# Performance work log

Measured on AMD Instinct MI355X. Metric: run time of the kernel, lower is better.

The kernel has to match this reference:

```python
import jax, jax.numpy as jnp
import numpy as np

WS = (4, 4, 4)          # window size (s, h, w)
NUM_HEADS = 6
DIM = 192               # kv channels C
CS = 2                  # channel_scale; q/out channels = DIM // CS
B = 256                 # num_windows * batch


def _rel_pos_index(ws):
    """Reproduces the module's relative_position_index buffer (shape [8shw, 2shw])."""
    s, h, w = ws
    cs = np.repeat(np.arange(s), 2)
    ch = np.repeat(np.arange(h), 2)
    cw = np.repeat(np.arange(w), 2)
    coords = np.stack(np.meshgrid(cs, ch, cw, indexing='ij'))   # (3, 2s, 2h, 2w)
    cf = coords.reshape(3, -1)                                   # (3, T), T = 8shw
    rel = cf[:, :, None] - cf[:, None, :]                        # (3, T, T)
    rel = rel[:, :, ::4]                                         # (3, T, T//4)
    rel = np.ascontiguousarray(rel.transpose(1, 2, 0))           # (T, T//4, 3)
    rel[:, :, 0] += s - 1
    rel[:, :, 1] += h - 1
    rel[:, :, 2] += w - 1
    rel[:, :, 0] *= 3 * h - 1
    rel[:, :, 1] *= 2 * h - 1
    return rel.sum(-1).astype(np.int32)                          # (T, T//4)


def setup_inputs() -> dict:
    key = jax.random.key(0)
    ks = jax.random.split(key, 9)
    s, h, w = WS
    qN = 8 * s * h * w          # 512 query tokens per window
    N = qN // 4                 # 128 key/value tokens per window
    C = DIM
    qC = DIM // CS
    table_len = (4 * s - 1) * (4 * h - 1) * (4 * w - 1)
    return {
        'kv': jax.random.normal(ks[0], (B, N, C), jnp.float32),
        'q': jax.random.normal(ks[1], (B, qN, qC), jnp.float32),
        'w_kv': jax.random.normal(ks[2], (C, 2 * C), jnp.float32) * 0.02,
        'b_kv': jnp.zeros((2 * C,), jnp.float32),
        'w_q': jax.random.normal(ks[3], (qC, C), jnp.float32) * 0.02,
        'b_q': jnp.zeros((C,), jnp.float32),
        'w_proj': jax.random.normal(ks[4], (C, qC), jnp.float32) * 0.02,
        'b_proj': jnp.zeros((qC,), jnp.float32),
        'bias_table': jax.random.normal(ks[5], (table_len, NUM_HEADS), jnp.float32) * 0.02,
        'rel_index': jnp.asarray(_rel_pos_index(WS)),
    }


def reference(kv, q, w_kv, b_kv, w_q, b_q, w_proj, b_proj, bias_table, rel_index):
    B_, N, C = kv.shape
    d = C // NUM_HEADS
    scale = d ** -0.5
    # project kv -> k, v : (B_, nH, N, d)
    kvp = (kv @ w_kv + b_kv).reshape(B_, N, 2, NUM_HEADS, d)
    k = kvp[:, :, 0].transpose(0, 2, 1, 3)
    v = kvp[:, :, 1].transpose(0, 2, 1, 3)
    # project q : (B_, nH, qN, d), pre-scaled
    qp = (q @ w_q + b_q).reshape(B_, -1, NUM_HEADS, d).transpose(0, 2, 1, 3) * scale
    attn = jnp.einsum('bhqd,bhkd->bhqk', qp, k)          # (B_, nH, qN, N)
    bias = bias_table[rel_index]                          # (qN, N, nH) gather
    attn = attn + bias.transpose(2, 0, 1)[None]           # + (1, nH, qN, N)
    attn = jax.nn.softmax(attn, axis=-1)
    out = jnp.einsum('bhqk,bhkd->bhqd', attn, v)          # (B_, nH, qN, d)
    out = out.transpose(0, 2, 1, 3).reshape(B_, -1, C)    # (B_, qN, C)
    return out @ w_proj + b_proj                          # (B_, qN, C//CS)
```

## Files before the change

### kernel.cpp

```cpp
#include <hip/hip_runtime.h>
#include <hip/hip_bf16.h>

#define B_    256
#define NKV   128
#define NQ    512
#define CDIM  192
#define QCDIM 96
#define NH    6
#define DH    32
#define SCALE 0.17677669529663687f

typedef __hip_bfloat16 bf16;
typedef __attribute__((ext_vector_type(8))) short s16x8;
typedef __attribute__((ext_vector_type(4))) float f32x4;
#define MFMA16(a, b, c) __builtin_amdgcn_mfma_f32_16x16x32_bf16(a, b, c, 0, 0, 0)

#define OFF_BIAS  0
#define OFF_WKVT  1572864
#define OFF_WQT   (OFF_WKVT + 147456)
#define OFF_WPT   (OFF_WQT + 36864)
#define OFF_O     2097152

#define LDS_K    0
#define LDS_VT   10240
#define LDS_STG  18944
#define LDS_P    18944
#define LDS_WKV  53760
#define LDS_WQ   53760
#define LDS_SQ   60416
#define LDS_TOT  79360

__global__ __launch_bounds__(256)
void precomp_bias(const float* __restrict__ bias_table, const int* __restrict__ rel_index,
                  float* __restrict__ biasM)
{
    const int i = blockIdx.x * 256 + threadIdx.x;
    const int h   = i >> 16;
    const int rem = i & 65535;
    biasM[i] = bias_table[rel_index[rem] * NH + h];
}

__global__ __launch_bounds__(256)
void precomp_w(const float* __restrict__ w_kv, const float* __restrict__ w_q,
               const float* __restrict__ w_proj,
               bf16* __restrict__ wkvT, bf16* __restrict__ wqT, bf16* __restrict__ wpT)
{
    const int i = blockIdx.x * 256 + threadIdx.x;
    if (i < NH * 64 * CDIM) {
        const int k = i % CDIM, jh = i / CDIM;
        const int j = jh & 63, h = jh >> 6;
        const int col = (j < DH) ? (h * DH + j) : (CDIM + h * DH + (j - DH));
        wkvT[i] = __float2bfloat16(w_kv[k * (2 * CDIM) + col]);
    } else if (i < NH * 64 * CDIM + NH * DH * QCDIM) {
        const int i2 = i - NH * 64 * CDIM;
        const int k = i2 % QCDIM, jh = i2 / QCDIM;
        const int j = jh & 31, h = jh >> 5;
        wqT[i2] = __float2bfloat16(w_q[k * CDIM + h * DH + j] * SCALE);
    } else {
        const int i3 = i - NH * 64 * CDIM - NH * DH * QCDIM;
        const int k = i3 % CDIM, n = i3 / CDIM;
        wpT[i3] = __float2bfloat16(w_proj[k * QCDIM + n]);
    }
}

__global__ __launch_bounds__(512, 4)
void attn_fused(const float* __restrict__ kv, const float* __restrict__ q,
                const float* __restrict__ b_kv, const float* __restrict__ b_q,
                const char* __restrict__ wsro, bf16* __restrict__ O)
{
    __shared__ __align__(16) char smem[LDS_TOT];
    bf16* sK   = (bf16*)(smem + LDS_K);
    bf16* sVT  = (bf16*)(smem + LDS_VT);
    bf16* sStg = (bf16*)(smem + LDS_STG);
    bf16* sP   = (bf16*)(smem + LDS_P);
    bf16* sWkv = (bf16*)(smem + LDS_WKV);
    bf16* sWq  = (bf16*)(smem + LDS_WQ);
    bf16* sQ   = (bf16*)(smem + LDS_SQ);

    const int b = blockIdx.x, h = blockIdx.y;
    const int t = threadIdx.x;
    const int wave = t >> 6, lane = t & 63, quad = lane >> 4, l16 = lane & 15;
    const f32x4 ZV = {0.f, 0.f, 0.f, 0.f};

    const float* biasM  = (const float*)(wsro + OFF_BIAS);
    const bf16*  wkvT_g = (const bf16*)(wsro + OFF_WKVT) + h * 64 * CDIM;
    const bf16*  wqT_g  = (const bf16*)(wsro + OFF_WQT) + h * DH * QCDIM;

    for (int f = t; f < 1536; f += 512) {
        const int j = f / 24, k8 = f % 24;
        *(uint4*)&sWkv[j * 200 + k8 * 8] = *(const uint4*)&wkvT_g[j * CDIM + k8 * 8];
    }

    f32x4 acc[4];
    #pragma unroll
    for (int i = 0; i < 4; ++i) acc[i] = ZV;

    for (int half = 0; half < 2; ++half) {
        for (int f = t; f < 3072; f += 512) {
            const int r = f / 24, c4 = f % 24;
            const float4 v = *(const float4*)&kv[((size_t)b * NKV + r) * CDIM + half * QCDIM + c4 * 4];
            __align__(8) bf16 tmp[4] = {__float2bfloat16(v.x), __float2bfloat16(v.y),
                                        __float2bfloat16(v.z), __float2bfloat16(v.w)};
            *(uint2*)&sStg[r * 104 + c4 * 4] = *(uint2*)tmp;
        }
        __syncthreads();
        #pragma unroll
        for (int kk = 0; kk < 3; ++kk) {
            const s16x8 a = *(const s16x8*)&sStg[(wave * 16 + l16) * 104 + kk * 32 + quad * 8];
            #pragma unroll
            for (int tl = 0; tl < 4; ++tl) {
                const s16x8 bb = *(const s16x8*)&sWkv[(tl * 16 + l16) * 200 + half * QCDIM + kk * 32 + quad * 8];
                acc[tl] = MFMA16(a, bb, acc[tl]);
            }
        }
        __syncthreads();
    }
    #pragma unroll
    for (int tl = 0; tl < 4; ++tl) {
        const int j = tl * 16 + l16;
        const float bkv = (j < DH) ? b_kv[h * DH + j] : b_kv[CDIM + h * DH + (j - DH)];
        #pragma unroll
        for (int r = 0; r < 4; ++r) {
            const int m = wave * 16 + quad * 4 + r;
            const float v = acc[tl][r] + bkv;
            if (j < DH) sK[m * 40 + j] = __float2bfloat16(v);
            else        sVT[(j - DH) * 136 + m] = __float2bfloat16(v);
        }
    }
    for (int f = t; f < 384; f += 512) {
        const int j = f / 12, k8 = f % 12;
        *(uint4*)&sWq[j * 104 + k8 * 8] = *(const uint4*)&wqT_g[j * QCDIM + k8 * 8];
    }

    for (int qc = 0; qc < 4; ++qc) {
        __syncthreads();
        for (int f = t; f < 3072; f += 512) {
            const int r = f / 24, c4 = f % 24;
            const float4 v = *(const float4*)&q[((size_t)b * NQ + qc * 128 + r) * QCDIM + c4 * 4];
            __align__(8) bf16 tmp[4] = {__float2bfloat16(v.x), __float2bfloat16(v.y),
                                        __float2bfloat16(v.z), __float2bfloat16(v.w)};
            *(uint2*)&sStg[r * 104 + c4 * 4] = *(uint2*)tmp;
        }
        __syncthreads();

        f32x4 qacc[2];
        qacc[0] = ZV; qacc[1] = ZV;
        #pragma unroll
        for (int kk = 0; kk < 3; ++kk) {
            const s16x8 a = *(const s16x8*)&sStg[(wave * 16 + l16) * 104 + kk * 32 + quad * 8];
            #pragma unroll
            for (int tl = 0; tl < 2; ++tl) {
                const s16x8 bb = *(const s16x8*)&sWq[(tl * 16 + l16) * 104 + kk * 32 + quad * 8];
                qacc[tl] = MFMA16(a, bb, qacc[tl]);
            }
        }
        #pragma unroll
        for (int tl = 0; tl < 2; ++tl) {
            const int cc = tl * 16 + l16;
            const float bq = b_q[h * DH + cc] * SCALE;
            #pragma unroll
            for (int r = 0; r < 4; ++r)
                sQ[(wave * 16 + quad * 4 + r) * 40 + cc] = __float2bfloat16(qacc[tl][r] + bq);
        }
        __syncthreads();

        f32x4 sacc[8];
        {
            const s16x8 a = *(const s16x8*)&sQ[(wave * 16 + l16) * 40 + quad * 8];
            #pragma unroll
            for (int tl = 0; tl < 8; ++tl) {
                const s16x8 bb = *(const s16x8*)&sK[(tl * 16 + l16) * 40 + quad * 8];
                sacc[tl] = MFMA16(a, bb, ZV);
            }
        }
        #pragma unroll
        for (int r = 0; r < 4; ++r) {
            const int qrow = qc * 128 + wave * 16 + quad * 4 + r;
            const float* brow = biasM + (((size_t)h * NQ + qrow) << 7) + l16;
            float v[8];
            float mx = -1e30f;
            #pragma unroll
            for (int tl = 0; tl < 8; ++tl) {
                v[tl] = sacc[tl][r] + brow[tl * 16];
                mx = fmaxf(mx, v[tl]);
            }
            #pragma unroll
            for (int off = 1; off < 16; off <<= 1) mx = fmaxf(mx, __shfl_xor(mx, off));
            float sum = 0.f;
            #pragma unroll
            for (int tl = 0; tl < 8; ++tl) { v[tl] = __expf(v[tl] - mx); sum += v[tl]; }
            #pragma unroll
            for (int off = 1; off < 16; off <<= 1) sum += __shfl_xor(sum, off);
            const float inv = 1.f / sum;
            const int prow = wave * 16 + quad * 4 + r;
            #pragma unroll
            for (int tl = 0; tl < 8; ++tl)
                sP[prow * 136 + tl * 16 + l16] = __float2bfloat16(v[tl] * inv);
        }
        __syncthreads();

        f32x4 oacc[2];
        oacc[0] = ZV; oacc[1] = ZV;
        #pragma unroll
        for (int kk = 0; kk < 4; ++kk) {
            const s16x8 a = *(const s16x8*)&sP[(wave * 16 + l16) * 136 + kk * 32 + quad * 8];
            #pragma unroll
            for (int tl = 0; tl < 2; ++tl) {
                const s16x8 bb = *(const s16x8*)&sVT[(tl * 16 + l16) * 136 + kk * 32 + quad * 8];
                oacc[tl] = MFMA16(a, bb, oacc[tl]);
            }
        }
        #pragma unroll
        for (int tl = 0; tl < 2; ++tl)
            #pragma unroll
            for (int r = 0; r < 4; ++r)
                O[((size_t)(b * NQ + qc * 128 + wave * 16 + quad * 4 + r)) * CDIM
                  + h * DH + tl * 16 + l16] = __float2bfloat16(oacc[tl][r]);
    }
}

__global__ __launch_bounds__(256)
void final_proj(const bf16* __restrict__ O, const bf16* __restrict__ wpT,
                const float* __restrict__ b_proj, float* __restrict__ out)
{
    __shared__ __align__(16) bf16 sO[64 * 200];
    __shared__ __align__(16) bf16 sW[96 * 200];
    const int row0 = blockIdx.x * 64;
    const int t = threadIdx.x;
    const int wave = t >> 6, lane = t & 63, quad = lane >> 4, l16 = lane & 15;
    const f32x4 ZV = {0.f, 0.f, 0.f, 0.f};

    for (int f = t; f < 1536; f += 256) {
        const int r = f / 24, c8 = f % 24;
        *(uint4*)&sO[r * 200 + c8 * 8] = *(const uint4*)&O[((size_t)(row0 + r)) * CDIM + c8 * 8];
    }
    for (int f = t; f < 2304; f += 256) {
        const int r = f / 24, c8 = f % 24;
        *(uint4*)&sW[r * 200 + c8 * 8] = *(const uint4*)&wpT[r * CDIM + c8 * 8];
    }
    __syncthreads();

    f32x4 acc[6];
    #pragma unroll
    for (int i = 0; i < 6; ++i) acc[i] = ZV;
    #pragma unroll
    for (int kk = 0; kk < 6; ++kk) {
        const s16x8 a = *(const s16x8*)&sO[(wave * 16 + l16) * 200 + kk * 32 + quad * 8];
        #pragma unroll
        for (int tl = 0; tl < 6; ++tl) {
            const s16x8 bb = *(const s16x8*)&sW[(tl * 16 + l16) * 200 + kk * 32 + quad * 8];
            acc[tl] = MFMA16(a, bb, acc[tl]);
        }
    }
    #pragma unroll
    for (int tl = 0; tl < 6; ++tl) {
        const float bp = b_proj[tl * 16 + l16];
        #pragma unroll
        for (int r = 0; r < 4; ++r)
            out[(size_t)(row0 + wave * 16 + quad * 4 + r) * QCDIM + tl * 16 + l16] = acc[tl][r] + bp;
    }
}

extern "C" void kernel_launch(void* const* d_in, const int* in_sizes, int n_in,
                              void* d_out, int out_size, void* d_ws, size_t ws_size,
                              hipStream_t stream)
{
    const float* kv       = (const float*)d_in[0];
    const float* q        = (const float*)d_in[1];
    const float* w_kv     = (const float*)d_in[2];
    const float* b_kv     = (const float*)d_in[3];
    const float* w_q      = (const float*)d_in[4];
    const float* b_q      = (const float*)d_in[5];
    const float* w_proj   = (const float*)d_in[6];
    const float* b_proj   = (const float*)d_in[7];
    const float* bias_tab = (const float*)d_in[8];
    const int*   rel_idx  = (const int*)d_in[9];
    char* ws = (char*)d_ws;

    precomp_bias<<<1536, 256, 0, stream>>>(bias_tab, rel_idx, (float*)(ws + OFF_BIAS));
    precomp_w<<<432, 256, 0, stream>>>(w_kv, w_q, w_proj,
                                       (bf16*)(ws + OFF_WKVT), (bf16*)(ws + OFF_WQT),
                                       (bf16*)(ws + OFF_WPT));
    attn_fused<<<dim3(B_, NH), 512, 0, stream>>>(kv, q, b_kv, b_q,
                                                 (const char*)ws, (bf16*)(ws + OFF_O));
    final_proj<<<(B_ * NQ) / 64, 256, 0, stream>>>((const bf16*)(ws + OFF_O),
                                                   (const bf16*)(ws + OFF_WPT),
                                                   b_proj, (float*)d_out);
}
```

Measured before the change: 257.5 us.

## Split KV projection into own kernel and fuse output projection into attention

Moves the K/V projection into a separate proj_kv kernel that writes bf16 K and transposed V to workspace. The attention kernel is reorganised to run one block per (window, query chunk) and loop over all heads, accumulating the output projection in registers. This removes the intermediate O buffer, the final_proj launch, and the q reload per head. The cost is that K, V and weights are read straight from global memory inside the MFMA loops instead of from LDS, and each block now does more serial work across heads.

Result: slower. 343.4 us (+33.3%).

```diff
diff --git a/kernel.cpp b/kernel.cpp
--- a/kernel.cpp
+++ b/kernel.cpp
@@ -19,16 +19,8 @@
 #define OFF_WKVT  1572864
 #define OFF_WQT   (OFF_WKVT + 147456)
 #define OFF_WPT   (OFF_WQT + 36864)
-#define OFF_O     2097152
-
-#define LDS_K    0
-#define LDS_VT   10240
-#define LDS_STG  18944
-#define LDS_P    18944
-#define LDS_WKV  53760
-#define LDS_WQ   53760
-#define LDS_SQ   60416
-#define LDS_TOT  79360
+#define OFF_KP    (OFF_WPT + 36864)
+#define OFF_VT    (OFF_KP + 12582912)
 
 __global__ __launch_bounds__(256)
 void precomp_bias(const float* __restrict__ bias_table, const int* __restrict__ rel_index,
@@ -46,137 +38,138 @@
                bf16* __restrict__ wkvT, bf16* __restrict__ wqT, bf16* __restrict__ wpT)
 {
     const int i = blockIdx.x * 256 + threadIdx.x;
-    if (i < NH * 64 * CDIM) {
-        const int k = i % CDIM, jh = i / CDIM;
-        const int j = jh & 63, h = jh >> 6;
-        const int col = (j < DH) ? (h * DH + j) : (CDIM + h * DH + (j - DH));
-        wkvT[i] = __float2bfloat16(w_kv[k * (2 * CDIM) + col]);
-    } else if (i < NH * 64 * CDIM + NH * DH * QCDIM) {
-        const int i2 = i - NH * 64 * CDIM;
-        const int k = i2 % QCDIM, jh = i2 / QCDIM;
-        const int j = jh & 31, h = jh >> 5;
-        wqT[i2] = __float2bfloat16(w_q[k * CDIM + h * DH + j] * SCALE);
+    if (i < 384 * CDIM) {
+        const int n = i / CDIM, k = i % CDIM;
+        wkvT[i] = __float2bfloat16(w_kv[k * (2 * CDIM) + n]);
+    } else if (i < 384 * CDIM + CDIM * QCDIM) {
+        const int i2 = i - 384 * CDIM;
+        const int n = i2 / QCDIM, k = i2 % QCDIM;
+        wqT[i2] = __float2bfloat16(w_q[k * CDIM + n] * SCALE);
     } else {
-        const int i3 = i - NH * 64 * CDIM - NH * DH * QCDIM;
-        const int k = i3 % CDIM, n = i3 / CDIM;
+        const int i3 = i - 384 * CDIM - CDIM * QCDIM;
+        const int n = i3 / CDIM, k = i3 % CDIM;
         wpT[i3] = __float2bfloat16(w_proj[k * QCDIM + n]);
     }
 }
 
+__global__ __launch_bounds__(512)
+void proj_kv(const float* __restrict__ kv, const float* __restrict__ b_kv,
+             const bf16* __restrict__ wkvT, bf16* __restrict__ Kp, bf16* __restrict__ VTp)
+{
+    __shared__ __align__(16) bf16 sA[128 * 200];
+    const int b = blockIdx.x, t = threadIdx.x;
+    const int w = t >> 6, lane = t & 63, quad = lane >> 4, l16 = lane & 15;
+    const f32x4 ZV = {0.f, 0.f, 0.f, 0.f};
+
+    for (int f = t; f < 6144; f += 512) {
+        const int r = f / 48, c4 = f % 48;
+        const float4 v = *(const float4*)&kv[((size_t)b * NKV + r) * CDIM + c4 * 4];
+        __align__(8) bf16 tmp[4] = {__float2bfloat16(v.x), __float2bfloat16(v.y),
+                                    __float2bfloat16(v.z), __float2bfloat16(v.w)};
+        *(uint2*)&sA[r * 200 + c4 * 4] = *(uint2*)tmp;
+    }
+    __syncthreads();
+
+    f32x4 acc[24];
+    #pragma unroll
+    for (int i = 0; i < 24; ++i) acc[i] = ZV;
+    for (int kk = 0; kk < 6; ++kk) {
+        const s16x8 a = *(const s16x8*)&sA[(w * 16 + l16) * 200 + kk * 32 + quad * 8];
+        #pragma unroll
+        for (int nt = 0; nt < 24; ++nt) {
+            const s16x8 bb = *(const s16x8*)&wkvT[(nt * 16 + l16) * CDIM + kk * 32 + quad * 8];
+            acc[nt] = MFMA16(a, bb, acc[nt]);
+        }
+    }
+    #pragma unroll
+    for (int nt = 0; nt < 24; ++nt) {
+        const int col = nt * 16 + l16;
+        const float bias = b_kv[col];
+        if (nt < 12) {
+            #pragma unroll
+            for (int r = 0; r < 4; ++r) {
+                const int m = w * 16 + quad * 4 + r;
+                Kp[((size_t)b * NKV + m) * CDIM + col] = __float2bfloat16(acc[nt][r] + bias);
+            }
+        } else {
+            const int j = col - CDIM;
+            __align__(8) bf16 tmp[4];
+            #pragma unroll
+            for (int r = 0; r < 4; ++r) tmp[r] = __float2bfloat16(acc[nt][r] + bias);
+            *(uint2*)&VTp[((size_t)b * CDIM + j) * NKV + w * 16 + quad * 4] = *(uint2*)tmp;
+        }
+    }
+}
+
 __global__ __launch_bounds__(512, 4)
-void attn_fused(const float* __restrict__ kv, const float* __restrict__ q,
-                const float* __restrict__ b_kv, const float* __restrict__ b_q,
-                const char* __restrict__ wsro, bf16* __restrict__ O)
-{
-    __shared__ __align__(16) char smem[LDS_TOT];
-    bf16* sK   = (bf16*)(smem + LDS_K);
-    bf16* sVT  = (bf16*)(smem + LDS_VT);
-    bf16* sStg = (bf16*)(smem + LDS_STG);
-    bf16* sP   = (bf16*)(smem + LDS_P);
-    bf16* sWkv = (bf16*)(smem + LDS_WKV);
-    bf16* sWq  = (bf16*)(smem + LDS_WQ);
-    bf16* sQ   = (bf16*)(smem + LDS_SQ);
-
-    const int b = blockIdx.x, h = blockIdx.y;
+void attn_fused(const float* __restrict__ q, const float* __restrict__ b_q,
+                const float* __restrict__ b_proj, const char* __restrict__ wsro,
+                float* __restrict__ out)
+{
+    __shared__ __align__(16) char smem[61440];
+    bf16* sQin = (bf16*)smem;
+    bf16* sP   = (bf16*)(smem + 26624);
+
+    const int b = blockIdx.x, qc = blockIdx.y;
     const int t = threadIdx.x;
-    const int wave = t >> 6, lane = t & 63, quad = lane >> 4, l16 = lane & 15;
+    const int w = t >> 6, lane = t & 63, quad = lane >> 4, l16 = lane & 15;
     const f32x4 ZV = {0.f, 0.f, 0.f, 0.f};
 
-    const float* biasM  = (const float*)(wsro + OFF_BIAS);
-    const bf16*  wkvT_g = (const bf16*)(wsro + OFF_WKVT) + h * 64 * CDIM;
-    const bf16*  wqT_g  = (const bf16*)(wsro + OFF_WQT) + h * DH * QCDIM;
-
-    for (int f = t; f < 1536; f += 512) {
-        const int j = f / 24, k8 = f % 24;
-        *(uint4*)&sWkv[j * 200 + k8 * 8] = *(const uint4*)&wkvT_g[j * CDIM + k8 * 8];
-    }
-
-    f32x4 acc[4];
-    #pragma unroll
-    for (int i = 0; i < 4; ++i) acc[i] = ZV;
-
-    for (int half = 0; half < 2; ++half) {
-        for (int f = t; f < 3072; f += 512) {
-            const int r = f / 24, c4 = f % 24;
-            const float4 v = *(const float4*)&kv[((size_t)b * NKV + r) * CDIM + half * QCDIM + c4 * 4];
-            __align__(8) bf16 tmp[4] = {__float2bfloat16(v.x), __float2bfloat16(v.y),
-                                        __float2bfloat16(v.z), __float2bfloat16(v.w)};
-            *(uint2*)&sStg[r * 104 + c4 * 4] = *(uint2*)tmp;
-        }
-        __syncthreads();
-        #pragma unroll
-        for (int kk = 0; kk < 3; ++kk) {
-            const s16x8 a = *(const s16x8*)&sStg[(wave * 16 + l16) * 104 + kk * 32 + quad * 8];
-            #pragma unroll
-            for (int tl = 0; tl < 4; ++tl) {
-                const s16x8 bb = *(const s16x8*)&sWkv[(tl * 16 + l16) * 200 + half * QCDIM + kk * 32 + quad * 8];
-                acc[tl] = MFMA16(a, bb, acc[tl]);
-            }
-        }
-        __syncthreads();
-    }
-    #pragma unroll
-    for (int tl = 0; tl < 4; ++tl) {
-        const int j = tl * 16 + l16;
-        const float bkv = (j < DH) ? b_kv[h * DH + j] : b_kv[CDIM + h * DH + (j - DH)];
-        #pragma unroll
-        for (int r = 0; r < 4; ++r) {
-            const int m = wave * 16 + quad * 4 + r;
-            const float v = acc[tl][r] + bkv;
-            if (j < DH) sK[m * 40 + j] = __float2bfloat16(v);
-            else        sVT[(j - DH) * 136 + m] = __float2bfloat16(v);
-        }
-    }
-    for (int f = t; f < 384; f += 512) {
-        const int j = f / 12, k8 = f % 12;
-        *(uint4*)&sWq[j * 104 + k8 * 8] = *(const uint4*)&wqT_g[j * QCDIM + k8 * 8];
-    }
-
-    for (int qc = 0; qc < 4; ++qc) {
-        __syncthreads();
-        for (int f = t; f < 3072; f += 512) {
-            const int r = f / 24, c4 = f % 24;
-            const float4 v = *(const float4*)&q[((size_t)b * NQ + qc * 128 + r) * QCDIM + c4 * 4];
-            __align__(8) bf16 tmp[4] = {__float2bfloat16(v.x), __float2bfloat16(v.y),
-                                        __float2bfloat16(v.z), __float2bfloat16(v.w)};
-            *(uint2*)&sStg[r * 104 + c4 * 4] = *(uint2*)tmp;
-        }
-        __syncthreads();
-
+    const float* biasM = (const float*)(wsro + OFF_BIAS);
+    const bf16*  wqT   = (const bf16*)(wsro + OFF_WQT);
+    const bf16*  wpT   = (const bf16*)(wsro + OFF_WPT);
+    const bf16*  Kp    = (const bf16*)(wsro + OFF_KP) + (size_t)b * NKV * CDIM;
+    const bf16*  VTp   = (const bf16*)(wsro + OFF_VT) + (size_t)b * CDIM * NKV;
+
+    for (int f = t; f < 3072; f += 512) {
+        const int r = f / 24, c4 = f % 24;
+        const float4 v = *(const float4*)&q[((size_t)b * NQ + qc * 128 + r) * QCDIM + c4 * 4];
+        __align__(8) bf16 tmp[4] = {__float2bfloat16(v.x), __float2bfloat16(v.y),
+                                    __float2bfloat16(v.z), __float2bfloat16(v.w)};
+        *(uint2*)&sQin[r * 104 + c4 * 4] = *(uint2*)tmp;
+    }
+    __syncthreads();
+
+    bf16* myP = sP + w * 16 * 136;
+
+    f32x4 outacc[6];
+    #pragma unroll
+    for (int i = 0; i < 6; ++i) outacc[i] = ZV;
+
+    for (int h = 0; h < NH; ++h) {
         f32x4 qacc[2];
         qacc[0] = ZV; qacc[1] = ZV;
         #pragma unroll
         for (int kk = 0; kk < 3; ++kk) {
-            const s16x8 a = *(const s16x8*)&sStg[(wave * 16 + l16) * 104 + kk * 32 + quad * 8];
+            const s16x8 a = *(const s16x8*)&sQin[(w * 16 + l16) * 104 + kk * 32 + quad * 8];
             #pragma unroll
             for (int tl = 0; tl < 2; ++tl) {
-                const s16x8 bb = *(const s16x8*)&sWq[(tl * 16 + l16) * 104 + kk * 32 + quad * 8];
+                const s16x8 bb = *(const s16x8*)&wqT[(h * DH + tl * 16 + l16) * QCDIM + kk * 32 + quad * 8];
                 qacc[tl] = MFMA16(a, bb, qacc[tl]);
             }
         }
         #pragma unroll
         for (int tl = 0; tl < 2; ++tl) {
-            const int cc = tl * 16 + l16;
-            const float bq = b_q[h * DH + cc] * SCALE;
+            const float bq = b_q[h * DH + tl * 16 + l16] * SCALE;
             #pragma unroll
             for (int r = 0; r < 4; ++r)
-                sQ[(wave * 16 + quad * 4 + r) * 40 + cc] = __float2bfloat16(qacc[tl][r] + bq);
-        }
-        __syncthreads();
-
+                myP[(quad * 4 + r) * 136 + tl * 16 + l16] = __float2bfloat16(qacc[tl][r] + bq);
+        }
+        __builtin_amdgcn_wave_barrier();
+
+        const s16x8 aQ = *(const s16x8*)&myP[l16 * 136 + quad * 8];
         f32x4 sacc[8];
-        {
-            const s16x8 a = *(const s16x8*)&sQ[(wave * 16 + l16) * 40 + quad * 8];
-            #pragma unroll
-            for (int tl = 0; tl < 8; ++tl) {
-                const s16x8 bb = *(const s16x8*)&sK[(tl * 16 + l16) * 40 + quad * 8];
-                sacc[tl] = MFMA16(a, bb, ZV);
-            }
-        }
+        #pragma unroll
+        for (int tl = 0; tl < 8; ++tl) {
+            const s16x8 bb = *(const s16x8*)&Kp[(size_t)(tl * 16 + l16) * CDIM + h * DH + quad * 8];
+            sacc[tl] = MFMA16(aQ, bb, ZV);
+        }
+        __builtin_amdgcn_wave_barrier();
+
         #pragma unroll
         for (int r = 0; r < 4; ++r) {
-            const int qrow = qc * 128 + wave * 16 + quad * 4 + r;
-            const float* brow = biasM + (((size_t)h * NQ + qrow) << 7) + l16;
+            const int qrow = qc * 128 + w * 16 + quad * 4 + r;
+            const float* brow = biasM + ((size_t)h * NQ + qrow) * NKV + l16;
             float v[8];
             float mx = -1e30f;
             #pragma unroll
@@ -192,72 +185,48 @@
             #pragma unroll
             for (int off = 1; off < 16; off <<= 1) sum += __shfl_xor(sum, off);
             const float inv = 1.f / sum;
-            const int prow = wave * 16 + quad * 4 + r;
             #pragma unroll
             for (int tl = 0; tl < 8; ++tl)
-                sP[prow * 136 + tl * 16 + l16] = __float2bfloat16(v[tl] * inv);
-        }
-        __syncthreads();
+                myP[(quad * 4 + r) * 136 + tl * 16 + l16] = __float2bfloat16(v[tl] * inv);
+        }
+        __builtin_amdgcn_wave_barrier();
 
         f32x4 oacc[2];
         oacc[0] = ZV; oacc[1] = ZV;
         #pragma unroll
         for (int kk = 0; kk < 4; ++kk) {
-            const s16x8 a = *(const s16x8*)&sP[(wave * 16 + l16) * 136 + kk * 32 + quad * 8];
+            const s16x8 aP = *(const s16x8*)&myP[l16 * 136 + kk * 32 + quad * 8];
             #pragma unroll
             for (int tl = 0; tl < 2; ++tl) {
-                const s16x8 bb = *(const s16x8*)&sVT[(tl * 16 + l16) * 136 + kk * 32 + quad * 8];
-                oacc[tl] = MFMA16(a, bb, oacc[tl]);
-            }
-        }
+                const s16x8 bb = *(const s16x8*)&VTp[(size_t)(h * DH + tl * 16 + l16) * NKV + kk * 32 + quad * 8];
+                oacc[tl] = MFMA16(aP, bb, oacc[tl]);
+            }
+        }
+        __builtin_amdgcn_wave_barrier();
+
         #pragma unroll
         for (int tl = 0; tl < 2; ++tl)
             #pragma unroll
             for (int r = 0; r < 4; ++r)
-                O[((size_t)(b * NQ + qc * 128 + wave * 16 + quad * 4 + r)) * CDIM
-                  + h * DH + tl * 16 + l16] = __float2bfloat16(oacc[tl][r]);
-    }
-}
-
-__global__ __launch_bounds__(256)
-void final_proj(const bf16* __restrict__ O, const bf16* __restrict__ wpT,
-                const float* __restrict__ b_proj, float* __restrict__ out)
-{
-    __shared__ __align__(16) bf16 sO[64 * 200];
-    __shared__ __align__(16) bf16 sW[96 * 200];
-    const int row0 = blockIdx.x * 64;
-    const int t = threadIdx.x;
-    const int wave = t >> 6, lane = t & 63, quad = lane >> 4, l16 = lane & 15;
-    const f32x4 ZV = {0.f, 0.f, 0.f, 0.f};
-
-    for (int f = t; f < 1536; f += 256) {
-        const int r = f / 24, c8 = f % 24;
-        *(uint4*)&sO[r * 200 + c8 * 8] = *(const uint4*)&O[((size_t)(row0 + r)) * CDIM + c8 * 8];
-    }
-    for (int f = t; f < 2304; f += 256) {
-        const int r = f / 24, c8 = f % 24;
-        *(uint4*)&sW[r * 200 + c8 * 8] = *(const uint4*)&wpT[r * CDIM + c8 * 8];
-    }
-    __syncthreads();
-
-    f32x4 acc[6];
-    #pragma unroll
-    for (int i = 0; i < 6; ++i) acc[i] = ZV;
-    #pragma unroll
-    for (int kk = 0; kk < 6; ++kk) {
-        const s16x8 a = *(const s16x8*)&sO[(wave * 16 + l16) * 200 + kk * 32 + quad * 8];
-        #pragma unroll
-        for (int tl = 0; tl < 6; ++tl) {
-            const s16x8 bb = *(const s16x8*)&sW[(tl * 16 + l16) * 200 + kk * 32 + quad * 8];
-            acc[tl] = MFMA16(a, bb, acc[tl]);
-        }
-    }
-    #pragma unroll
-    for (int tl = 0; tl < 6; ++tl) {
-        const float bp = b_proj[tl * 16 + l16];
+                myP[(quad * 4 + r) * 136 + tl * 16 + l16] = __float2bfloat16(oacc[tl][r]);
+        __builtin_amdgcn_wave_barrier();
+
+        const s16x8 aO = *(const s16x8*)&myP[l16 * 136 + quad * 8];
+        #pragma unroll
+        for (int tn = 0; tn < 6; ++tn) {
+            const s16x8 bb = *(const s16x8*)&wpT[(tn * 16 + l16) * CDIM + h * DH + quad * 8];
+            outacc[tn] = MFMA16(aO, bb, outacc[tn]);
+        }
+        __builtin_amdgcn_wave_barrier();
+    }
+
+    #pragma unroll
+    for (int tn = 0; tn < 6; ++tn) {
+        const float bp = b_proj[tn * 16 + l16];
         #pragma unroll
         for (int r = 0; r < 4; ++r)
-            out[(size_t)(row0 + wave * 16 + quad * 4 + r) * QCDIM + tl * 16 + l16] = acc[tl][r] + bp;
+            out[((size_t)b * NQ + qc * 128 + w * 16 + quad * 4 + r) * QCDIM + tn * 16 + l16]
+                = outacc[tn][r] + bp;
     }
 }
 
@@ -281,9 +250,8 @@
     precomp_w<<<432, 256, 0, stream>>>(w_kv, w_q, w_proj,
                                        (bf16*)(ws + OFF_WKVT), (bf16*)(ws + OFF_WQT),
                                        (bf16*)(ws + OFF_WPT));
-    attn_fused<<<dim3(B_, NH), 512, 0, stream>>>(kv, q, b_kv, b_q,
-                                                 (const char*)ws, (bf16*)(ws + OFF_O));
-    final_proj<<<(B_ * NQ) / 64, 256, 0, stream>>>((const bf16*)(ws + OFF_O),
-                                                   (const bf16*)(ws + OFF_WPT),
-                                                   b_proj, (float*)d_out);
-}
+    proj_kv<<<B_, 512, 0, stream>>>(kv, b_kv, (const bf16*)(ws + OFF_WKVT),
+                                    (bf16*)(ws + OFF_KP), (bf16*)(ws + OFF_VT));
+    attn_fused<<<dim3(B_, 4), 512, 0, stream>>>(q, b_q, b_proj, (const char*)ws,
+                                                (float*)d_out);
+}
```
